# Kernel tuning notes

Measured on AMD Instinct MI355X. Metric: run time of the kernel, lower is better.

The kernel has to match this reference:

```python
import jax, jax.numpy as jnp
import numpy as np

G = 512          # fine grid size
N_FINE = 150000  # target active fine voxels
THRESH = 0.8     # scn PPN Selection threshold


def _keys(c, g):
    c = c.astype(np.int64)
    return (c[:, 0] * g + c[:, 1]) * g + c[:, 2]


def _neighbors(coords, g):
    # coords: [N,3] int. Returns [N,27] neighbor indices; N == missing sentinel.
    keys = _keys(coords, g)
    order = np.argsort(keys)
    skeys = keys[order]
    N = coords.shape[0]
    offs = np.array([[dx, dy, dz] for dx in (-1, 0, 1) for dy in (-1, 0, 1) for dz in (-1, 0, 1)], np.int64)
    nbr = np.full((N, 27), N, np.int64)
    for k, o in enumerate(offs):
        nc = coords + o
        valid = np.all((nc >= 0) & (nc < g), axis=1)
        nk = _keys(np.clip(nc, 0, g - 1), g)
        pos = np.clip(np.searchsorted(skeys, nk), 0, N - 1)
        found = valid & (skeys[pos] == nk)
        nbr[:, k] = np.where(found, order[pos], N)
    return nbr


def _lookup(query, table, g):
    keys = _keys(table, g)
    order = np.argsort(keys)
    sk = keys[order]
    qk = _keys(query, g)
    pos = np.clip(np.searchsorted(sk, qk), 0, len(sk) - 1)
    return order[pos]


def setup_inputs() -> dict:
    rng = np.random.default_rng(0)
    pts = rng.integers(0, G, size=(2 * N_FINE, 3))
    fine = np.unique(pts, axis=0)[:N_FINE]              # stride-1 active sites
    mid = np.unique(fine // 4, axis=0)                  # stride-4 active sites
    coarse = np.unique(fine // 16, axis=0)              # stride-16 active sites
    N1, N2, N3 = coarse.shape[0], mid.shape[0], fine.shape[0]

    nbr1 = _neighbors(coarse, G // 16)
    nbr2 = _neighbors(mid, G // 4)
    nbr3 = _neighbors(fine, G)
    parent2 = _lookup(mid // 4, coarse, G // 16)        # middle voxel -> coarse parent
    parent3 = _lookup(fine // 4, mid, G // 4)           # fine voxel -> middle parent

    key = jax.random.key(0)
    ks = jax.random.split(key, 12)

    def w(k, shape):
        fan_in = shape[0] * shape[1]
        return jax.random.normal(k, shape, jnp.float32) / np.sqrt(fan_in)

    def coords4(c):  # prepend batch-id column (all batch 0) like get_spatial_locations
        return jnp.asarray(np.concatenate([c, np.zeros((c.shape[0], 1), c.dtype)], 1), jnp.int32)

    return {
        'feat1': jax.random.normal(ks[0], (N1, 80), jnp.float32),
        'feat2': jax.random.normal(ks[1], (N2, 48), jnp.float32),
        'feat3': jax.random.normal(ks[2], (N3, 16), jnp.float32),
        'W1': w(ks[3], (27, 80, 80)), 'W1s': w(ks[4], (27, 80, 2)),
        'W2': w(ks[5], (27, 48, 48)), 'W2s': w(ks[6], (27, 48, 2)),
        'W3': w(ks[7], (27, 16, 16)), 'W3p': w(ks[8], (27, 16, 3)),
        'W3s': w(ks[9], (27, 16, 2)), 'W3t': w(ks[10], (27, 16, 5)),
        'nbr1': jnp.asarray(nbr1, jnp.int32), 'nbr2': jnp.asarray(nbr2, jnp.int32),
        'nbr3': jnp.asarray(nbr3, jnp.int32),
        'parent2': jnp.asarray(parent2, jnp.int32), 'parent3': jnp.asarray(parent3, jnp.int32),
        'coords1': coords4(coarse), 'coords2': coords4(mid),
    }


def subconv(feat, nbr, W):
    # Submanifold 3^3 conv: out only at active sites; missing neighbors -> 0 (padded row).
    fp = jnp.concatenate([feat, jnp.zeros((1, feat.shape[1]), feat.dtype)], 0)
    g = fp[nbr]                               # [N, 27, Cin]
    return jnp.einsum('nkc,kcd->nd', g, W)    # [N, Cout]


def reference(feat1, feat2, feat3, W1, W1s, W2, W2s, W3, W3p, W3s, W3t,
              nbr1, nbr2, nbr3, parent2, parent3, coords1, coords2):
    # --- PPN1 on coarsest decoder features ---
    y = subconv(feat1, nbr1, W1)
    s1 = subconv(y, nbr1, W1s)                              # ppn1_scores [N1,2]
    mask1 = (jax.nn.softmax(s1, axis=1)[:, 1:] > THRESH).astype(feat1.dtype)  # Selection
    att1 = mask1[parent2]                                   # UnPooling x2: coarse -> middle
    # --- PPN2 on middle decoder features ---
    y2 = subconv(feat2 * att1, nbr2, W2)                    # Multiply then conv
    s2 = subconv(y2, nbr2, W2s)                             # ppn2_scores [N2,2]
    mask2 = (jax.nn.softmax(s2, axis=1)[:, 1:] > THRESH).astype(feat1.dtype)
    att2 = mask2[parent3]                                   # UnPooling x2: middle -> fine
    # --- PPN3 on finest decoder features ---
    z = subconv(feat3 * att2, nbr3, W3)
    pixel_pred = subconv(z, nbr3, W3p)                      # [N3,3]
    scores = subconv(z, nbr3, W3s)                          # [N3,2]
    ptype = subconv(z, nbr3, W3t)                           # [N3,5]
    points = jnp.concatenate([pixel_pred, scores, ptype], axis=1)
    ppn1 = jnp.concatenate([coords1.astype(jnp.float32), s1], axis=1)
    ppn2 = jnp.concatenate([coords2.astype(jnp.float32), s2], axis=1)
    return points, ppn1, ppn2, mask1, mask2
```

## Files before the change

### kernel.cpp

```cpp
#include <hip/hip_runtime.h>

typedef _Float16 f16;
typedef _Float16 f16x8 __attribute__((ext_vector_type(8)));
typedef float f32x4 __attribute__((ext_vector_type(4)));

#define LN4 1.3862943611198906f

__device__ __forceinline__ void gl_lds16(const void* g, void* l) {
    typedef unsigned int u32;
    __builtin_amdgcn_global_load_lds(
        (const __attribute__((address_space(1))) u32*)(g),
        (__attribute__((address_space(3))) u32*)(l), 16, 0, 0);
}

__global__ __launch_bounds__(256) void prep_w1_kernel(
    const float* __restrict__ W, f16* __restrict__ dst)
{
    const int CIN = 80, COUT = 80;
    int total = COUT * 28 * CIN;
    for (int i = blockIdx.x * 256 + threadIdx.x; i < total; i += gridDim.x * 256) {
        int d = i / (28 * CIN);
        int rem = i - d * (28 * CIN);
        int tap = rem / CIN;
        int c = rem - tap * CIN;
        float v = (tap < 27) ? W[(size_t)(tap * CIN + c) * COUT + d] : 0.f;
        f16 h = (f16)v;
        size_t base = (size_t)d * (28 * 2 * CIN) + (size_t)tap * (2 * CIN);
        dst[base + c] = h;
        dst[base + CIN + c] = (f16)(v - (float)h);
    }
}

template<int CIN, int COUT>
__global__ __launch_bounds__(256) void prep_frag(
    const float* __restrict__ Wa, int ca, f16* __restrict__ FT)
{
    constexpr int KB = (2 * CIN) / 32;
    int total = 14 * KB * 1024;
    for (int i = blockIdx.x * 256 + threadIdx.x; i < total; i += gridDim.x * 256) {
        int j = i & 7;
        int lane = (i >> 3) & 63;
        int term = (i >> 9) & 1;
        int kbp = i >> 10;
        int kb = kbp % KB, p = kbp / KB;
        int k = kb * 32 + ((lane >> 4) * 8) + j;
        int ts = (k >= CIN) ? 1 : 0;
        int kk = k - ts * CIN;
        int tap = 2 * p + ts;
        int col = lane & 15;
        float v = 0.f;
        if (tap < 27 && col < COUT && col < ca) {
            int kc = tap * CIN + kk;
            v = Wa[(size_t)kc * ca + col];
        }
        f16 h = (f16)v;
        FT[i] = term ? (f16)(v - (float)h) : h;
    }
}

__global__ __launch_bounds__(256) void split80_kernel(
    const float* __restrict__ f, f16* __restrict__ Fc, int N)
{
    int i = blockIdx.x * 256 + threadIdx.x;
    if (i >= (N + 1) * 80) return;
    int n = i / 80, c = i - n * 80;
    float v = (n < N) ? f[i] : 0.f;
    f16 h = (f16)v;
    Fc[(size_t)n * 160 + c] = h;
    Fc[(size_t)n * 160 + 80 + c] = (f16)(v - (float)h);
}

__global__ __launch_bounds__(256) void ppn_finalize_kernel(
    const int* __restrict__ coords, const float* __restrict__ s,
    float* __restrict__ ppn, float* __restrict__ mask, int N)
{
    int n = blockIdx.x * 256 + threadIdx.x;
    if (n >= N) return;
    float s0 = s[(size_t)n * 2 + 0], s1 = s[(size_t)n * 2 + 1];
    ppn[(size_t)n * 6 + 0] = (float)coords[(size_t)n * 4 + 0];
    ppn[(size_t)n * 6 + 1] = (float)coords[(size_t)n * 4 + 1];
    ppn[(size_t)n * 6 + 2] = (float)coords[(size_t)n * 4 + 2];
    ppn[(size_t)n * 6 + 3] = (float)coords[(size_t)n * 4 + 3];
    ppn[(size_t)n * 6 + 4] = s0;
    ppn[(size_t)n * 6 + 5] = s1;
    mask[n] = (s1 - s0 > LN4) ? 1.0f : 0.0f;
}

__global__ __launch_bounds__(256) void gate_kernel(
    const float* __restrict__ mask, const int* __restrict__ parent,
    float* __restrict__ act, int N)
{
    int i = blockIdx.x * 256 + threadIdx.x;
    if (i < N) act[i] = mask[parent[i]];
}

template<bool FSRC>
__global__ __launch_bounds__(256) void expand_kernel(
    const void* __restrict__ src, const int* __restrict__ nbr,
    int* __restrict__ flag, int N)
{
    int m = blockIdx.x * 256 + threadIdx.x;
    if (m >= N) return;
    bool a = FSRC ? (((const float*)src)[m] != 0.f) : (((const int*)src)[m] != 0);
    if (!a) return;
    #pragma unroll 1
    for (int t = 0; t < 27; ++t) {
        int idx = nbr[(size_t)m * 27 + t];
        if (idx < N) flag[idx] = 1;
    }
}

__global__ __launch_bounds__(256) void compact_kernel(
    const int* __restrict__ flag, int* __restrict__ list,
    int* __restrict__ cnt, int N)
{
    int i = blockIdx.x * 256 + threadIdx.x;
    int lane = threadIdx.x & 63;
    bool f = (i < N) && (flag[i] != 0);
    unsigned long long m = __ballot(f);
    int base = 0;
    if (lane == 0 && m) base = atomicAdd(cnt, __popcll(m));
    base = __shfl(base, 0);
    if (f) list[base + __popcll(m & ((1ull << lane) - 1ull))] = i;
}

__global__ __launch_bounds__(256, 3) void conv80_y(
    const f16* __restrict__ F, const int* __restrict__ nbr,
    const f16* __restrict__ WT, f16* __restrict__ Y, int N, int nTiles)
{
    constexpr int RE = 160, CPT = 20, CPR = 40, PB = 640, KB = 5, BM = 64;
    __shared__ __align__(16) char BS[80 * PB];

    const int t = threadIdx.x;
    const int lane = t & 63;
    const int l16 = lane & 15;
    const int quad = lane >> 4;
    const int wv = t >> 6;

    int q8 = (nTiles + 7) >> 3;
    int tile = (blockIdx.x & 7) * q8 + (blockIdx.x >> 3);
    if (tile >= nTiles) return;
    const int m0 = tile * BM;
    const int grow = m0 + wv * 16 + l16;

    f16x8 ahA[KB], alA[KB], ahB[KB], alB[KB];

    auto loadA = [&](int p, f16x8 (&ah)[KB], f16x8 (&al)[KB]) {
        int i0 = N, i1 = N;
        if (grow < N) {
            i0 = nbr[(size_t)grow * 27 + 2 * p];
            if (2 * p + 1 < 27) i1 = nbr[(size_t)grow * 27 + 2 * p + 1];
        }
        #pragma unroll
        for (int kb = 0; kb < KB; ++kb) {
            int ko = kb * 32 + quad * 8;
            int ts = ko >= 80;
            int c2 = ko - (ts ? 80 : 0);
            const f16* ap = F + (size_t)(ts ? i1 : i0) * RE + c2;
            ah[kb] = *(const f16x8*)ap;
            al[kb] = *(const f16x8*)(ap + 80);
        }
    };

    auto stageB = [&](int p) {
        for (int i = t; i < 80 * CPR; i += 256) {
            int d = i / CPR, cs = i - d * CPR;
            int c = (cs & ~7) | ((cs ^ d) & 7);
            int tp = c / CPT, cc = c - tp * CPT;
            gl_lds16((const char*)WT + (((size_t)d * 28 + 2 * p + tp) * RE + cc * 8) * 2,
                     BS + (size_t)i * 16);
        }
    };

    f32x4 acc[5];
    #pragma unroll
    for (int ct = 0; ct < 5; ++ct) acc[ct] = (f32x4){0.f, 0.f, 0.f, 0.f};

    auto compute = [&](f16x8 (&ah)[KB], f16x8 (&al)[KB]) {
        #pragma unroll
        for (int kb = 0; kb < KB; ++kb) {
            int ko = kb * 32 + quad * 8;
            int ts = ko >= 80;
            int c2 = ko - (ts ? 80 : 0);
            int ch = ts * CPT + c2 / 8;
            int chl = ch + 10;
            #pragma unroll
            for (int ct = 0; ct < 5; ++ct) {
                int drow = ct * 16 + l16;
                int sb = (ch & ~7) | ((ch ^ drow) & 7);
                int sbl = (chl & ~7) | ((chl ^ drow) & 7);
                f16x8 bh = *(const f16x8*)(BS + drow * PB + sb * 16);
                f16x8 bl = *(const f16x8*)(BS + drow * PB + sbl * 16);
                acc[ct] = __builtin_amdgcn_mfma_f32_16x16x32_f16(ah[kb], bh, acc[ct], 0, 0, 0);
                acc[ct] = __builtin_amdgcn_mfma_f32_16x16x32_f16(al[kb], bh, acc[ct], 0, 0, 0);
                acc[ct] = __builtin_amdgcn_mfma_f32_16x16x32_f16(ah[kb], bl, acc[ct], 0, 0, 0);
            }
        }
    };

    loadA(0, ahA, alA);
    #pragma unroll 1
    for (int p = 0; p < 14; p += 2) {
        __syncthreads();
        stageB(p);
        loadA(p + 1, ahB, alB);
        __syncthreads();
        compute(ahA, alA);

        __syncthreads();
        stageB(p + 1);
        if (p + 2 < 14) loadA(p + 2, ahA, alA);
        __syncthreads();
        compute(ahB, alB);
    }

    #pragma unroll
    for (int ct = 0; ct < 5; ++ct) {
        #pragma unroll
        for (int r = 0; r < 4; ++r) {
            int row = m0 + wv * 16 + quad * 4 + r;
            if (row < N) {
                int d = ct * 16 + l16;
                float v = acc[ct][r];
                f16 h = (f16)v;
                Y[(size_t)row * RE + d] = h;
                Y[(size_t)row * RE + 80 + d] = (f16)(v - (float)h);
            }
        }
    }
}

template<int CIN, int COUT>
__global__ __launch_bounds__(256) void score_tile(
    const f16* __restrict__ Y, const int* __restrict__ nbr,
    const f16* __restrict__ FT, float* __restrict__ S, int N, int nTiles)
{
    constexpr int RE = 2 * CIN;
    constexpr int KB = RE / 32;

    const int t = threadIdx.x;
    const int lane = t & 63;
    const int l16 = lane & 15;
    const int quad = lane >> 4;
    const int wv = t >> 6;

    int q8 = (nTiles + 7) >> 3;
    int tile = (blockIdx.x & 7) * q8 + (blockIdx.x >> 3);
    if (tile >= nTiles) return;
    const int m0 = tile * 64;
    const int grow = m0 + wv * 16 + l16;
    const bool gv = grow < N;

    f32x4 acc = (f32x4){0.f, 0.f, 0.f, 0.f};

    #pragma unroll 1
    for (int p = 0; p < 14; ++p) {
        int i0 = N, i1 = N;
        if (gv) {
            i0 = nbr[(size_t)grow * 27 + 2 * p];
            if (2 * p + 1 < 27) i1 = nbr[(size_t)grow * 27 + 2 * p + 1];
        }
        #pragma unroll
        for (int kb = 0; kb < KB; ++kb) {
            int ko = kb * 32 + quad * 8;
            int ts = ko >= CIN;
            int c2 = ko - (ts ? CIN : 0);
            const f16* ap = Y + (size_t)(ts ? i1 : i0) * RE + c2;
            f16x8 ah = *(const f16x8*)ap;
            f16x8 al = *(const f16x8*)(ap + CIN);
            const f16* fb = FT + (size_t)(p * KB + kb) * 1024 + lane * 8;
            f16x8 bh = *(const f16x8*)fb;
            f16x8 bl = *(const f16x8*)(fb + 512);
            acc = __builtin_amdgcn_mfma_f32_16x16x32_f16(ah, bh, acc, 0, 0, 0);
            acc = __builtin_amdgcn_mfma_f32_16x16x32_f16(al, bh, acc, 0, 0, 0);
            acc = __builtin_amdgcn_mfma_f32_16x16x32_f16(ah, bl, acc, 0, 0, 0);
        }
    }

    if (l16 < COUT) {
        #pragma unroll
        for (int r = 0; r < 4; ++r) {
            int row = m0 + wv * 16 + quad * 4 + r;
            if (row < N) S[(size_t)row * COUT + l16] = acc[r];
        }
    }
}

__global__ __launch_bounds__(256) void lvl2_compute(
    const float* __restrict__ feat2, const int* __restrict__ nbr2,
    const float* __restrict__ act, const float* __restrict__ W2,
    const float* __restrict__ W2s, float* __restrict__ s2,
    const int* __restrict__ list, const int* __restrict__ cnt, int N)
{
    const int lane = threadIdx.x & 63;
    const int wid0 = (blockIdx.x * 256 + threadIdx.x) >> 6;
    const int nw = (gridDim.x * 256) >> 6;
    const int count = *cnt;
    const int c = lane;

    for (int w = wid0; w < count; w += nw) {
        const int n = list[w];
        int ld = N;
        if (lane < 27) ld = nbr2[(size_t)n * 27 + lane];
        bool valid = (lane < 27) && (ld < N);
        float a = valid ? act[ld] : 0.f;
        unsigned long long actm = __ballot(a != 0.f);
        unsigned long long vmask = __ballot(valid);

        float acc = 0.f;
        unsigned long long m = actm;
        while (m) {
            int t = __ffsll(m) - 1; m &= m - 1;
            int idx = __shfl(ld, t);
            const float4* f4 = (const float4*)(feat2 + (size_t)idx * 48);
            const float* wgt = W2 + (size_t)t * 48 * 48;
            #pragma unroll
            for (int q = 0; q < 12; ++q) {
                float4 fv = f4[q];
                if (c < 48) {
                    acc += fv.x * wgt[(4 * q + 0) * 48 + c];
                    acc += fv.y * wgt[(4 * q + 1) * 48 + c];
                    acc += fv.z * wgt[(4 * q + 2) * 48 + c];
                    acc += fv.w * wgt[(4 * q + 3) * 48 + c];
                }
            }
        }

        m = vmask;
        while (m) {
            int t = __ffsll(m) - 1; m &= m - 1;
            int idx = __shfl(ld, t);
            float p0 = 0.f, p1 = 0.f;
            if (c < 48) {
                float2 wv2 = ((const float2*)W2s)[(size_t)(26 - t) * 48 + c];
                p0 = acc * wv2.x; p1 = acc * wv2.y;
            }
            #pragma unroll
            for (int s = 32; s; s >>= 1) { p0 += __shfl_down(p0, s); p1 += __shfl_down(p1, s); }
            if (lane == 0) {
                atomicAdd(&s2[(size_t)idx * 2 + 0], p0);
                atomicAdd(&s2[(size_t)idx * 2 + 1], p1);
            }
        }
    }
}

__global__ __launch_bounds__(256) void lvl3_z_compute(
    const float* __restrict__ feat3, const int* __restrict__ nbr3,
    const float* __restrict__ act, const float* __restrict__ W3,
    float* __restrict__ z, const int* __restrict__ list,
    const int* __restrict__ cnt, int N)
{
    const int lane = threadIdx.x & 63;
    const int wid0 = (blockIdx.x * 256 + threadIdx.x) >> 6;
    const int nw = (gridDim.x * 256) >> 6;
    const int count = *cnt;
    const int c = lane;

    for (int w = wid0; w < count; w += nw) {
        const int n = list[w];
        int ld = N;
        if (lane < 27) ld = nbr3[(size_t)n * 27 + lane];
        bool valid = (lane < 27) && (ld < N);
        float a = valid ? act[ld] : 0.f;
        unsigned long long m = __ballot(a != 0.f);

        float acc = 0.f;
        while (m) {
            int t = __ffsll(m) - 1; m &= m - 1;
            int idx = __shfl(ld, t);
            const float4* f4 = (const float4*)(feat3 + (size_t)idx * 16);
            const float* wgt = W3 + (size_t)t * 256;
            #pragma unroll
            for (int q = 0; q < 4; ++q) {
                float4 fv = f4[q];
                if (c < 16) {
                    acc += fv.x * wgt[(4 * q + 0) * 16 + c];
                    acc += fv.y * wgt[(4 * q + 1) * 16 + c];
                    acc += fv.z * wgt[(4 * q + 2) * 16 + c];
                    acc += fv.w * wgt[(4 * q + 3) * 16 + c];
                }
            }
        }
        if (lane < 16) z[(size_t)n * 16 + lane] = acc;
    }
}

__global__ __launch_bounds__(256) void lvl3_pts_compute(
    const float* __restrict__ z, const int* __restrict__ zflag,
    const int* __restrict__ nbr3,
    const float* __restrict__ Wp, const float* __restrict__ Ws,
    const float* __restrict__ Wt, float* __restrict__ points,
    const int* __restrict__ list, const int* __restrict__ cnt, int N)
{
    const int lane = threadIdx.x & 63;
    const int wid0 = (blockIdx.x * 256 + threadIdx.x) >> 6;
    const int nw = (gridDim.x * 256) >> 6;
    const int count = *cnt;
    const int c = lane;

    for (int w = wid0; w < count; w += nw) {
        const int n = list[w];
        int ld = N;
        if (lane < 27) ld = nbr3[(size_t)n * 27 + lane];
        bool valid = (lane < 27) && (ld < N);
        int zf = valid ? zflag[ld] : 0;
        unsigned long long m = __ballot(zf != 0);

        float acc = 0.f;
        while (m) {
            int t = __ffsll(m) - 1; m &= m - 1;
            int idx = __shfl(ld, t);
            const float4* z4 = (const float4*)(z + (size_t)idx * 16);
            #pragma unroll
            for (int q = 0; q < 4; ++q) {
                float4 zv = z4[q];
                if (c < 10) {
                    #pragma unroll
                    for (int j = 0; j < 4; ++j) {
                        int k = 4 * q + j;
                        int kc = t * 16 + k;
                        float wv = (c < 3) ? Wp[(size_t)kc * 3 + c]
                                 : (c < 5) ? Ws[(size_t)kc * 2 + (c - 3)]
                                           : Wt[(size_t)kc * 5 + (c - 5)];
                        float zj = (j == 0) ? zv.x : (j == 1) ? zv.y : (j == 2) ? zv.z : zv.w;
                        acc += zj * wv;
                    }
                }
            }
        }
        if (lane < 10) points[(size_t)n * 10 + lane] = acc;
    }
}

extern "C" void kernel_launch(void* const* d_in, const int* in_sizes, int n_in,
                              void* d_out, int out_size, void* d_ws, size_t ws_size,
                              hipStream_t stream)
{
    const float* feat1 = (const float*)d_in[0];
    const float* feat2 = (const float*)d_in[1];
    const float* feat3 = (const float*)d_in[2];
    const float* W1    = (const float*)d_in[3];
    const float* W1s   = (const float*)d_in[4];
    const float* W2    = (const float*)d_in[5];
    const float* W2s   = (const float*)d_in[6];
    const float* W3    = (const float*)d_in[7];
    const float* W3p   = (const float*)d_in[8];
    const float* W3s   = (const float*)d_in[9];
    const float* W3t   = (const float*)d_in[10];
    const int* nbr1    = (const int*)d_in[11];
    const int* nbr2    = (const int*)d_in[12];
    const int* nbr3    = (const int*)d_in[13];
    const int* parent2 = (const int*)d_in[14];
    const int* parent3 = (const int*)d_in[15];
    const int* coords1 = (const int*)d_in[16];
    const int* coords2 = (const int*)d_in[17];

    const int N1 = in_sizes[0] / 80;
    const int N2 = in_sizes[1] / 48;
    const int N3 = in_sizes[2] / 16;

    float* out = (float*)d_out;
    float* o_points = out;
    float* o_ppn1   = o_points + (size_t)N3 * 10;
    float* o_ppn2   = o_ppn1 + (size_t)N1 * 6;
    float* o_mask1  = o_ppn2 + (size_t)N2 * 6;
    float* o_mask2  = o_mask1 + (size_t)N1;

    char* wp = (char*)d_ws;
    auto alloc = [&](size_t bytes) -> char* {
        char* r = wp; wp += (bytes + 255) & ~(size_t)255; return r;
    };
    f16*   WT1   = (f16*)alloc((size_t)80 * 28 * 160 * 2);
    f16*   FT1   = (f16*)alloc((size_t)14 * 5 * 1024 * 2);
    f16*   Fa    = (f16*)alloc((size_t)(N1 + 1) * 160 * 2);
    f16*   Y1    = (f16*)alloc((size_t)(N1 + 1) * 160 * 2);
    float* s1    = (float*)alloc((size_t)(N1 + 1) * 2 * 4);
    float* s2    = (float*)alloc((size_t)(N2 + 1) * 2 * 4);
    float* act2  = (float*)alloc((size_t)N2 * 4);
    float* act3  = (float*)alloc((size_t)N3 * 4);
    int*   flag2 = (int*)alloc((size_t)N2 * 4);
    int*   list2 = (int*)alloc((size_t)N2 * 4);
    int*   flagz = (int*)alloc((size_t)N3 * 4);
    int*   listz = (int*)alloc((size_t)N3 * 4);
    int*   flagp = (int*)alloc((size_t)N3 * 4);
    int*   listp = (int*)alloc((size_t)N3 * 4);
    float* zbuf  = (float*)alloc((size_t)N3 * 16 * 4);
    int*   cnts  = (int*)alloc(3 * 4);

    auto cdiv = [](long long a, long long b) { return (int)((a + b - 1) / b); };

    hipMemsetAsync(s1, 0, (size_t)(N1 + 1) * 2 * 4, stream);
    hipMemsetAsync(s2, 0, (size_t)(N2 + 1) * 2 * 4, stream);
    hipMemsetAsync(Y1 + (size_t)N1 * 160, 0, 160 * 2, stream);
    hipMemsetAsync(flag2, 0, (size_t)N2 * 4, stream);
    hipMemsetAsync(flagz, 0, (size_t)N3 * 4, stream);
    hipMemsetAsync(flagp, 0, (size_t)N3 * 4, stream);
    hipMemsetAsync(zbuf, 0, (size_t)N3 * 16 * 4, stream);
    hipMemsetAsync(cnts, 0, 3 * 4, stream);
    hipMemsetAsync(o_points, 0, (size_t)N3 * 10 * 4, stream);

    prep_w1_kernel<<<700, 256, 0, stream>>>(W1, WT1);
    prep_frag<80, 2><<<cdiv(14 * 5 * 1024, 256), 256, 0, stream>>>(W1s, 2, FT1);
    split80_kernel<<<cdiv((size_t)(N1 + 1) * 80, 256), 256, 0, stream>>>(feat1, Fa, N1);
    {
        int T = cdiv(N1, 64);
        dim3 grid(8 * cdiv(T, 8));
        conv80_y<<<grid, 256, 0, stream>>>(Fa, nbr1, WT1, Y1, N1, T);
        score_tile<80, 2><<<grid, 256, 0, stream>>>(Y1, nbr1, FT1, s1, N1, T);
    }
    ppn_finalize_kernel<<<cdiv(N1, 256), 256, 0, stream>>>(coords1, s1, o_ppn1, o_mask1, N1);

    gate_kernel<<<cdiv(N2, 256), 256, 0, stream>>>(o_mask1, parent2, act2, N2);
    expand_kernel<true><<<cdiv(N2, 256), 256, 0, stream>>>(act2, nbr2, flag2, N2);
    compact_kernel<<<cdiv(N2, 256), 256, 0, stream>>>(flag2, list2, &cnts[0], N2);
    lvl2_compute<<<2048, 256, 0, stream>>>(feat2, nbr2, act2, W2, W2s, s2,
                                           list2, &cnts[0], N2);
    ppn_finalize_kernel<<<cdiv(N2, 256), 256, 0, stream>>>(coords2, s2, o_ppn2, o_mask2, N2);

    gate_kernel<<<cdiv(N3, 256), 256, 0, stream>>>(o_mask2, parent3, act3, N3);
    expand_kernel<true><<<cdiv(N3, 256), 256, 0, stream>>>(act3, nbr3, flagz, N3);
    compact_kernel<<<cdiv(N3, 256), 256, 0, stream>>>(flagz, listz, &cnts[1], N3);
    lvl3_z_compute<<<2048, 256, 0, stream>>>(feat3, nbr3, act3, W3, zbuf,
                                             listz, &cnts[1], N3);
    expand_kernel<false><<<cdiv(N3, 256), 256, 0, stream>>>(flagz, nbr3, flagp, N3);
    compact_kernel<<<cdiv(N3, 256), 256, 0, stream>>>(flagp, listp, &cnts[2], N3);
    lvl3_pts_compute<<<2048, 256, 0, stream>>>(zbuf, flagz, nbr3, W3p, W3s, W3t,
                                               o_points, listp, &cnts[2], N3);
}
```

Measured before the change: 400.3 us.

## Run level-2 PPN conv on dense MFMA tile kernels instead of sparse scalar path

Makes the MFMA-based gather conv and score kernels generic over the input channel count and uses them for the middle level (48 channels). This replaces the gate/expand/compact pipeline and the per-wave scalar FMA kernel that used atomic scatter. Gating is folded into the fp16 hi/lo split kernel, which zeroes features whose coarse parent mask is off. It also shares workspace buffers between stages to cut allocations and memsets. The trade-off is that all middle voxels are now computed densely instead of only the active ones, and the split-fp16 emulation with three MFMAs per product changes numerics slightly.

```diff
diff --git a/kernel.cpp b/kernel.cpp
--- a/kernel.cpp
+++ b/kernel.cpp
@@ -13,19 +13,20 @@
         (__attribute__((address_space(3))) u32*)(l), 16, 0, 0);
 }
 
-__global__ __launch_bounds__(256) void prep_w1_kernel(
+template<int CIN>
+__global__ __launch_bounds__(256) void prep_wt(
     const float* __restrict__ W, f16* __restrict__ dst)
 {
-    const int CIN = 80, COUT = 80;
-    int total = COUT * 28 * CIN;
+    const int RE = 2 * CIN;
+    int total = CIN * 28 * CIN;
     for (int i = blockIdx.x * 256 + threadIdx.x; i < total; i += gridDim.x * 256) {
         int d = i / (28 * CIN);
         int rem = i - d * (28 * CIN);
         int tap = rem / CIN;
         int c = rem - tap * CIN;
-        float v = (tap < 27) ? W[(size_t)(tap * CIN + c) * COUT + d] : 0.f;
+        float v = (tap < 27) ? W[(size_t)(tap * CIN + c) * CIN + d] : 0.f;
         f16 h = (f16)v;
-        size_t base = (size_t)d * (28 * 2 * CIN) + (size_t)tap * (2 * CIN);
+        size_t base = (size_t)d * (28 * RE) + (size_t)tap * RE;
         dst[base + c] = h;
         dst[base + CIN + c] = (f16)(v - (float)h);
     }
@@ -58,16 +59,22 @@
     }
 }
 
-__global__ __launch_bounds__(256) void split80_kernel(
-    const float* __restrict__ f, f16* __restrict__ Fc, int N)
+template<int CIN>
+__global__ __launch_bounds__(256) void split_gated(
+    const float* __restrict__ f, const float* __restrict__ mask,
+    const int* __restrict__ parent, f16* __restrict__ Fc, int N)
 {
     int i = blockIdx.x * 256 + threadIdx.x;
-    if (i >= (N + 1) * 80) return;
-    int n = i / 80, c = i - n * 80;
-    float v = (n < N) ? f[i] : 0.f;
+    if (i >= (N + 1) * CIN) return;
+    int n = i / CIN, c = i - n * CIN;
+    float v = 0.f;
+    if (n < N) {
+        bool a = parent ? (mask[parent[n]] != 0.f) : true;
+        v = a ? f[i] : 0.f;
+    }
     f16 h = (f16)v;
-    Fc[(size_t)n * 160 + c] = h;
-    Fc[(size_t)n * 160 + 80 + c] = (f16)(v - (float)h);
+    Fc[(size_t)n * (2 * CIN) + c] = h;
+    Fc[(size_t)n * (2 * CIN) + CIN + c] = (f16)(v - (float)h);
 }
 
 __global__ __launch_bounds__(256) void ppn_finalize_kernel(
@@ -124,12 +131,18 @@
     if (f) list[base + __popcll(m & ((1ull << lane) - 1ull))] = i;
 }
 
-__global__ __launch_bounds__(256, 3) void conv80_y(
+template<int CIN>
+__global__ __launch_bounds__(256, 3) void conv_tile(
     const f16* __restrict__ F, const int* __restrict__ nbr,
     const f16* __restrict__ WT, f16* __restrict__ Y, int N, int nTiles)
 {
-    constexpr int RE = 160, CPT = 20, CPR = 40, PB = 640, KB = 5, BM = 64;
-    __shared__ __align__(16) char BS[80 * PB];
+    constexpr int RE = 2 * CIN;
+    constexpr int KB = RE / 32;
+    constexpr int CT = CIN / 16;
+    constexpr int CPT = RE / 8;
+    constexpr int CPR = 2 * CPT;
+    constexpr int PB = CPR * 16;
+    __shared__ __align__(16) char BS[CIN * PB];
 
     const int t = threadIdx.x;
     const int lane = t & 63;
@@ -140,7 +153,7 @@
     int q8 = (nTiles + 7) >> 3;
     int tile = (blockIdx.x & 7) * q8 + (blockIdx.x >> 3);
     if (tile >= nTiles) return;
-    const int m0 = tile * BM;
+    const int m0 = tile * 64;
     const int grow = m0 + wv * 16 + l16;
 
     f16x8 ahA[KB], alA[KB], ahB[KB], alB[KB];
@@ -154,16 +167,16 @@
         #pragma unroll
         for (int kb = 0; kb < KB; ++kb) {
             int ko = kb * 32 + quad * 8;
-            int ts = ko >= 80;
-            int c2 = ko - (ts ? 80 : 0);
+            int ts = ko >= CIN;
+            int c2 = ko - (ts ? CIN : 0);
             const f16* ap = F + (size_t)(ts ? i1 : i0) * RE + c2;
             ah[kb] = *(const f16x8*)ap;
-            al[kb] = *(const f16x8*)(ap + 80);
+            al[kb] = *(const f16x8*)(ap + CIN);
         }
     };
 
     auto stageB = [&](int p) {
-        for (int i = t; i < 80 * CPR; i += 256) {
+        for (int i = t; i < CIN * CPR; i += 256) {
             int d = i / CPR, cs = i - d * CPR;
             int c = (cs & ~7) | ((cs ^ d) & 7);
             int tp = c / CPT, cc = c - tp * CPT;
@@ -172,20 +185,20 @@
         }
     };
 
-    f32x4 acc[5];
+    f32x4 acc[CT];
     #pragma unroll
-    for (int ct = 0; ct < 5; ++ct) acc[ct] = (f32x4){0.f, 0.f, 0.f, 0.f};
+    for (int ct = 0; ct < CT; ++ct) acc[ct] = (f32x4){0.f, 0.f, 0.f, 0.f};
 
     auto compute = [&](f16x8 (&ah)[KB], f16x8 (&al)[KB]) {
         #pragma unroll
         for (int kb = 0; kb < KB; ++kb) {
             int ko = kb * 32 + quad * 8;
-            int ts = ko >= 80;
-            int c2 = ko - (ts ? 80 : 0);
+            int ts = ko >= CIN;
+            int c2 = ko - (ts ? CIN : 0);
             int ch = ts * CPT + c2 / 8;
-            int chl = ch + 10;
+            int chl = ch + CIN / 8;
             #pragma unroll
-            for (int ct = 0; ct < 5; ++ct) {
+            for (int ct = 0; ct < CT; ++ct) {
                 int drow = ct * 16 + l16;
                 int sb = (ch & ~7) | ((ch ^ drow) & 7);
                 int sbl = (chl & ~7) | ((chl ^ drow) & 7);
@@ -215,7 +228,7 @@
     }
 
     #pragma unroll
-    for (int ct = 0; ct < 5; ++ct) {
+    for (int ct = 0; ct < CT; ++ct) {
         #pragma unroll
         for (int r = 0; r < 4; ++r) {
             int row = m0 + wv * 16 + quad * 4 + r;
@@ -224,7 +237,7 @@
                 float v = acc[ct][r];
                 f16 h = (f16)v;
                 Y[(size_t)row * RE + d] = h;
-                Y[(size_t)row * RE + 80 + d] = (f16)(v - (float)h);
+                Y[(size_t)row * RE + CIN + d] = (f16)(v - (float)h);
             }
         }
     }
@@ -282,65 +295,6 @@
         for (int r = 0; r < 4; ++r) {
             int row = m0 + wv * 16 + quad * 4 + r;
             if (row < N) S[(size_t)row * COUT + l16] = acc[r];
-        }
-    }
-}
-
-__global__ __launch_bounds__(256) void lvl2_compute(
-    const float* __restrict__ feat2, const int* __restrict__ nbr2,
-    const float* __restrict__ act, const float* __restrict__ W2,
-    const float* __restrict__ W2s, float* __restrict__ s2,
-    const int* __restrict__ list, const int* __restrict__ cnt, int N)
-{
-    const int lane = threadIdx.x & 63;
-    const int wid0 = (blockIdx.x * 256 + threadIdx.x) >> 6;
-    const int nw = (gridDim.x * 256) >> 6;
-    const int count = *cnt;
-    const int c = lane;
-
-    for (int w = wid0; w < count; w += nw) {
-        const int n = list[w];
-        int ld = N;
-        if (lane < 27) ld = nbr2[(size_t)n * 27 + lane];
-        bool valid = (lane < 27) && (ld < N);
-        float a = valid ? act[ld] : 0.f;
-        unsigned long long actm = __ballot(a != 0.f);
-        unsigned long long vmask = __ballot(valid);
-
-        float acc = 0.f;
-        unsigned long long m = actm;
-        while (m) {
-            int t = __ffsll(m) - 1; m &= m - 1;
-            int idx = __shfl(ld, t);
-            const float4* f4 = (const float4*)(feat2 + (size_t)idx * 48);
-            const float* wgt = W2 + (size_t)t * 48 * 48;
-            #pragma unroll
-            for (int q = 0; q < 12; ++q) {
-                float4 fv = f4[q];
-                if (c < 48) {
-                    acc += fv.x * wgt[(4 * q + 0) * 48 + c];
-                    acc += fv.y * wgt[(4 * q + 1) * 48 + c];
-                    acc += fv.z * wgt[(4 * q + 2) * 48 + c];
-                    acc += fv.w * wgt[(4 * q + 3) * 48 + c];
-                }
-            }
-        }
-
-        m = vmask;
-        while (m) {
-            int t = __ffsll(m) - 1; m &= m - 1;
-            int idx = __shfl(ld, t);
-            float p0 = 0.f, p1 = 0.f;
-            if (c < 48) {
-                float2 wv2 = ((const float2*)W2s)[(size_t)(26 - t) * 48 + c];
-                p0 = acc * wv2.x; p1 = acc * wv2.y;
-            }
-            #pragma unroll
-            for (int s = 32; s; s >>= 1) { p0 += __shfl_down(p0, s); p1 += __shfl_down(p1, s); }
-            if (lane == 0) {
-                atomicAdd(&s2[(size_t)idx * 2 + 0], p0);
-                atomicAdd(&s2[(size_t)idx * 2 + 1], p1);
-            }
         }
     }
 }
@@ -471,60 +425,74 @@
     auto alloc = [&](size_t bytes) -> char* {
         char* r = wp; wp += (bytes + 255) & ~(size_t)255; return r;
     };
-    f16*   WT1   = (f16*)alloc((size_t)80 * 28 * 160 * 2);
-    f16*   FT1   = (f16*)alloc((size_t)14 * 5 * 1024 * 2);
-    f16*   Fa    = (f16*)alloc((size_t)(N1 + 1) * 160 * 2);
-    f16*   Y1    = (f16*)alloc((size_t)(N1 + 1) * 160 * 2);
-    float* s1    = (float*)alloc((size_t)(N1 + 1) * 2 * 4);
-    float* s2    = (float*)alloc((size_t)(N2 + 1) * 2 * 4);
-    float* act2  = (float*)alloc((size_t)N2 * 4);
-    float* act3  = (float*)alloc((size_t)N3 * 4);
-    int*   flag2 = (int*)alloc((size_t)N2 * 4);
-    int*   list2 = (int*)alloc((size_t)N2 * 4);
-    int*   flagz = (int*)alloc((size_t)N3 * 4);
-    int*   listz = (int*)alloc((size_t)N3 * 4);
-    int*   flagp = (int*)alloc((size_t)N3 * 4);
-    int*   listp = (int*)alloc((size_t)N3 * 4);
-    float* zbuf  = (float*)alloc((size_t)N3 * 16 * 4);
-    int*   cnts  = (int*)alloc(3 * 4);
+    auto A256 = [](size_t b) { return (b + 255) & ~(size_t)255; };
+
+    f16*   WT1 = (f16*)alloc((size_t)80 * 28 * 160 * 2);
+    f16*   WT2 = (f16*)alloc((size_t)48 * 28 * 96 * 2);
+    f16*   FT1 = (f16*)alloc((size_t)14 * 5 * 1024 * 2);
+    f16*   FT2 = (f16*)alloc((size_t)14 * 3 * 1024 * 2);
+    float* s1  = (float*)alloc((size_t)N1 * 2 * 4);
+    float* s2  = (float*)alloc((size_t)N2 * 2 * 4);
+    float* act3 = (float*)alloc((size_t)N3 * 4);
+    int*   cnts = (int*)alloc(2 * 4);
+
+    size_t e1 = (size_t)(N1 + 1) * 160, e2 = (size_t)(N2 + 1) * 96;
+    size_t eF = e1 > e2 ? e1 : e2;
+    f16* Fa = (f16*)alloc(eF * 2);
+
+    size_t l3b = 4 * A256((size_t)N3 * 4) + A256((size_t)N3 * 16 * 4);
+    size_t eY = eF * 2 > l3b ? eF * 2 : l3b;
+    char* Yu = alloc(eY);
+    f16* Y = (f16*)Yu;
+    char* q3 = Yu;
+    int*   flagz = (int*)q3; q3 += A256((size_t)N3 * 4);
+    int*   listz = (int*)q3; q3 += A256((size_t)N3 * 4);
+    int*   flagp = (int*)q3; q3 += A256((size_t)N3 * 4);
+    int*   listp = (int*)q3; q3 += A256((size_t)N3 * 4);
+    float* zbuf  = (float*)q3;
 
     auto cdiv = [](long long a, long long b) { return (int)((a + b - 1) / b); };
 
-    hipMemsetAsync(s1, 0, (size_t)(N1 + 1) * 2 * 4, stream);
-    hipMemsetAsync(s2, 0, (size_t)(N2 + 1) * 2 * 4, stream);
-    hipMemsetAsync(Y1 + (size_t)N1 * 160, 0, 160 * 2, stream);
-    hipMemsetAsync(flag2, 0, (size_t)N2 * 4, stream);
+    hipMemsetAsync(Y + (size_t)N1 * 160, 0, 160 * 2, stream);
+    hipMemsetAsync(Y + (size_t)N2 * 96, 0, 96 * 2, stream);
+    hipMemsetAsync(cnts, 0, 2 * 4, stream);
+    hipMemsetAsync(o_points, 0, (size_t)N3 * 10 * 4, stream);
+
+    prep_wt<80><<<700, 256, 0, stream>>>(W1, WT1);
+    prep_wt<48><<<cdiv(48 * 28 * 48, 256), 256, 0, stream>>>(W2, WT2);
+    prep_frag<80, 2><<<cdiv(14 * 5 * 1024, 256), 256, 0, stream>>>(W1s, 2, FT1);
+    prep_frag<48, 2><<<cdiv(14 * 3 * 1024, 256), 256, 0, stream>>>(W2s, 2, FT2);
+
+    {
+        int T = cdiv(N1, 64);
+        dim3 grid(8 * cdiv(T, 8));
+        split_gated<80><<<cdiv((size_t)(N1 + 1) * 80, 256), 256, 0, stream>>>(
+            feat1, nullptr, nullptr, Fa, N1);
+        conv_tile<80><<<grid, 256, 0, stream>>>(Fa, nbr1, WT1, Y, N1, T);
+        score_tile<80, 2><<<grid, 256, 0, stream>>>(Y, nbr1, FT1, s1, N1, T);
+    }
+    ppn_finalize_kernel<<<cdiv(N1, 256), 256, 0, stream>>>(coords1, s1, o_ppn1, o_mask1, N1);
+
+    {
+        int T = cdiv(N2, 64);
+        dim3 grid(8 * cdiv(T, 8));
+        split_gated<48><<<cdiv((size_t)(N2 + 1) * 48, 256), 256, 0, stream>>>(
+            feat2, o_mask1, parent2, Fa, N2);
+        conv_tile<48><<<grid, 256, 0, stream>>>(Fa, nbr2, WT2, Y, N2, T);
+        score_tile<48, 2><<<grid, 256, 0, stream>>>(Y, nbr2, FT2, s2, N2, T);
+    }
+    ppn_finalize_kernel<<<cdiv(N2, 256), 256, 0, stream>>>(coords2, s2, o_ppn2, o_mask2, N2);
+
     hipMemsetAsync(flagz, 0, (size_t)N3 * 4, stream);
     hipMemsetAsync(flagp, 0, (size_t)N3 * 4, stream);
     hipMemsetAsync(zbuf, 0, (size_t)N3 * 16 * 4, stream);
-    hipMemsetAsync(cnts, 0, 3 * 4, stream);
-    hipMemsetAsync(o_points, 0, (size_t)N3 * 10 * 4, stream);
-
-    prep_w1_kernel<<<700, 256, 0, stream>>>(W1, WT1);
-    prep_frag<80, 2><<<cdiv(14 * 5 * 1024, 256), 256, 0, stream>>>(W1s, 2, FT1);
-    split80_kernel<<<cdiv((size_t)(N1 + 1) * 80, 256), 256, 0, stream>>>(feat1, Fa, N1);
-    {
-        int T = cdiv(N1, 64);
-        dim3 grid(8 * cdiv(T, 8));
-        conv80_y<<<grid, 256, 0, stream>>>(Fa, nbr1, WT1, Y1, N1, T);
-        score_tile<80, 2><<<grid, 256, 0, stream>>>(Y1, nbr1, FT1, s1, N1, T);
-    }
-    ppn_finalize_kernel<<<cdiv(N1, 256), 256, 0, stream>>>(coords1, s1, o_ppn1, o_mask1, N1);
-
-    gate_kernel<<<cdiv(N2, 256), 256, 0, stream>>>(o_mask1, parent2, act2, N2);
-    expand_kernel<true><<<cdiv(N2, 256), 256, 0, stream>>>(act2, nbr2, flag2, N2);
-    compact_kernel<<<cdiv(N2, 256), 256, 0, stream>>>(flag2, list2, &cnts[0], N2);
-    lvl2_compute<<<2048, 256, 0, stream>>>(feat2, nbr2, act2, W2, W2s, s2,
-                                           list2, &cnts[0], N2);
-    ppn_finalize_kernel<<<cdiv(N2, 256), 256, 0, stream>>>(coords2, s2, o_ppn2, o_mask2, N2);
-
     gate_kernel<<<cdiv(N3, 256), 256, 0, stream>>>(o_mask2, parent3, act3, N3);
     expand_kernel<true><<<cdiv(N3, 256), 256, 0, stream>>>(act3, nbr3, flagz, N3);
-    compact_kernel<<<cdiv(N3, 256), 256, 0, stream>>>(flagz, listz, &cnts[1], N3);
+    compact_kernel<<<cdiv(N3, 256), 256, 0, stream>>>(flagz, listz, &cnts[0], N3);
     lvl3_z_compute<<<2048, 256, 0, stream>>>(feat3, nbr3, act3, W3, zbuf,
-                                             listz, &cnts[1], N3);
+                                             listz, &cnts[0], N3);
     expand_kernel<false><<<cdiv(N3, 256), 256, 0, stream>>>(flagz, nbr3, flagp, N3);
-    compact_kernel<<<cdiv(N3, 256), 256, 0, stream>>>(flagp, listp, &cnts[2], N3);
+    compact_kernel<<<cdiv(N3, 256), 256, 0, stream>>>(flagp, listp, &cnts[1], N3);
     lvl3_pts_compute<<<2048, 256, 0, stream>>>(zbuf, flagz, nbr3, W3p, W3s, W3t,
-                                               o_points, listp, &cnts[2], N3);
-}
+                                               o_points, listp, &cnts[1], N3);
+}
```

Result: no change. 403.9 us (+0.9%).
